# Performance work log

Hardware: AMD Instinct MI355X
Metric: run time of the kernel (lower is better)

## Reference

```python
import jax, jax.numpy as jnp
import numpy as np

N, E, IN_DIM, HID, H, D = 50000, 800000, 1280, 256, 4, 64  # gat_out_dim = H*D = HID
NEG_SLOPE = 0.2


def setup_inputs() -> dict:
    key = jax.random.key(0)
    ks = jax.random.split(key, 20)

    def lin(k, fi, fo):
        return (jax.random.normal(k, (fi, fo), jnp.float32) / np.float32(np.sqrt(fi)))

    inp = {
        "x": jax.random.normal(ks[0], (N, IN_DIM), jnp.float32),
        "edge_index": jax.random.randint(ks[1], (2, E), 0, N, dtype=jnp.int32),
        "enc_W": lin(ks[2], IN_DIM, HID), "enc_b": jnp.zeros((HID,), jnp.float32),
        "Wl0": lin(ks[3], HID, H * D), "bl0": jnp.zeros((H * D,), jnp.float32),
        "Wr0": lin(ks[4], HID, H * D), "br0": jnp.zeros((H * D,), jnp.float32),
        "att0": jax.random.normal(ks[5], (H, D), jnp.float32) / np.float32(np.sqrt(D)),
        "bias0": jnp.zeros((H * D,), jnp.float32),
        "Wl1": lin(ks[6], HID, H * D), "bl1": jnp.zeros((H * D,), jnp.float32),
        "Wr1": lin(ks[7], HID, H * D), "br1": jnp.zeros((H * D,), jnp.float32),
        "att1": jax.random.normal(ks[8], (H, D), jnp.float32) / np.float32(np.sqrt(D)),
        "bias1": jnp.zeros((H * D,), jnp.float32),
        "clf_W": lin(ks[9], HID, 1), "clf_b": jnp.zeros((1,), jnp.float32),
    }
    return inp


def gatv2_layer(x, src, dst, Wl, bl, Wr, br, att, bias):
    # x: [N, HID]; src/dst: [E'] with self-loops already appended
    xl = (x @ Wl + bl).reshape(N, H, D)  # source transform
    xr = (x @ Wr + br).reshape(N, H, D)  # target transform
    e = jax.nn.leaky_relu(xl[src] + xr[dst], NEG_SLOPE)   # [E', H, D]
    logits = jnp.einsum('ehd,hd->eh', e, att)              # [E', H]
    # segment softmax over destination nodes (every node has a self-loop)
    m = jax.ops.segment_max(logits, dst, num_segments=N)   # [N, H]
    a = jnp.exp(logits - m[dst])
    denom = jax.ops.segment_sum(a, dst, num_segments=N)
    alpha = a / (denom[dst] + 1e-16)                       # [E', H]
    out = jax.ops.segment_sum(xl[src] * alpha[:, :, None], dst, num_segments=N)
    out = out.reshape(N, H * D) + bias
    out = out + x  # residual (in_dim == out_features -> identity residual); dropout is eval-mode no-op
    return jax.nn.elu(out), alpha


def reference(x, edge_index, enc_W, enc_b, Wl0, bl0, Wr0, br0, att0, bias0,
              Wl1, bl1, Wr1, br1, att1, bias1, clf_W, clf_b):
    # add self loops (PyG GATv2Conv default)
    loops = jnp.arange(N, dtype=edge_index.dtype)
    src = jnp.concatenate([edge_index[0], loops])
    dst = jnp.concatenate([edge_index[1], loops])

    h = x @ enc_W + enc_b                                  # node encoder [N, HID]
    h, alpha0 = gatv2_layer(h, src, dst, Wl0, bl0, Wr0, br0, att0, bias0)
    h, alpha1 = gatv2_layer(h, src, dst, Wl1, bl1, Wr1, br1, att1, bias1)
    preds = (h @ clf_W + clf_b).squeeze(-1)                # [N]
    return preds, alpha0, alpha1
```

## Files before the change

### kernel.cpp

```cpp
#include <hip/hip_runtime.h>
#include <hip/hip_bf16.h>
#include <math.h>

#define N_NODES 50000
#define E_EDGES 800000
#define EP (E_EDGES + N_NODES)
#define IN_DIM 1280
#define HID 256
#define NHEAD 4
#define DHEAD 64
#define NEG_SLOPE 0.2f

typedef unsigned short ushort_t;
typedef __attribute__((ext_vector_type(8))) short short8;
typedef __attribute__((ext_vector_type(4))) float floatx4;

__device__ __forceinline__ void split_bf16(float x, ushort_t& hi, ushort_t& lo) {
  unsigned u = __float_as_uint(x);
  hi = (ushort_t)(u >> 16);
  float rem = x - __uint_as_float(u & 0xFFFF0000u);
  lo = (ushort_t)(__float_as_uint(rem) >> 16);
}

__device__ __forceinline__ void gload_lds16(const void* g, void* l) {
  __builtin_amdgcn_global_load_lds(
      (const __attribute__((address_space(1))) unsigned int*)g,
      (__attribute__((address_space(3))) unsigned int*)l, 16, 0, 0);
}


__global__ void hist_kernel(const int* __restrict__ ei, int* __restrict__ deg) {
  int e = blockIdx.x * blockDim.x + threadIdx.x;
  if (e >= EP) return;
  int dst = (e < E_EDGES) ? ei[E_EDGES + e] : (e - E_EDGES);
  atomicAdd(&deg[dst], 1);
}

__global__ __launch_bounds__(1024) void scan_kernel(int* __restrict__ dc, int* __restrict__ row_ptr) {
  __shared__ int wsum[16];
  int tid = threadIdx.x;
  int lane = tid & 63;
  int wid = tid >> 6;
  int running = 0;
  if (tid == 0) row_ptr[0] = 0;
  for (int base = 0; base < N_NODES; base += 1024) {
    int i = base + tid;
    int v = (i < N_NODES) ? dc[i] : 0;
    int s = v;
    #pragma unroll
    for (int off = 1; off < 64; off <<= 1) {
      int t = __shfl_up(s, off);
      if (lane >= off) s += t;
    }
    if (lane == 63) wsum[wid] = s;
    __syncthreads();
    if (wid == 0 && lane < 16) {
      int w = wsum[lane];
      #pragma unroll
      for (int off = 1; off < 16; off <<= 1) {
        int t = __shfl_up(w, off);
        if (lane >= off) w += t;
      }
      wsum[lane] = w;
    }
    __syncthreads();
    int woff = (wid > 0) ? wsum[wid - 1] : 0;
    int incl = running + woff + s;
    if (i < N_NODES) {
      row_ptr[i + 1] = incl;
      dc[i] = incl - v;
    }
    running += wsum[15];
    __syncthreads();
  }
}

__global__ void scatter_kernel(const int* __restrict__ ei, int* __restrict__ cursor,
                               int* __restrict__ csr_src, int* __restrict__ csr_eid) {
  int e = blockIdx.x * blockDim.x + threadIdx.x;
  if (e >= EP) return;
  int src, dst;
  if (e < E_EDGES) { src = ei[e]; dst = ei[E_EDGES + e]; }
  else             { src = dst = e - E_EDGES; }
  int pos = atomicAdd(&cursor[dst], 1);
  csr_src[pos] = src;
  csr_eid[pos] = e;
}

__global__ void wsplit_packed(const float* __restrict__ W, ushort_t* __restrict__ Ph,
                              ushort_t* __restrict__ Pl, int K, int Nc, int NcT, int colOff) {
  int idx = blockIdx.x * blockDim.x + threadIdx.x;
  if (idx >= K * Nc) return;
  int k = idx / Nc, n = idx - k * Nc;
  ushort_t hi, lo;
  split_bf16(W[idx], hi, lo);
  size_t pi = ((size_t)(k >> 3) * NcT + colOff + n) * 8 + (k & 7);
  Ph[pi] = hi;
  Pl[pi] = lo;
}

__device__ __forceinline__ void split_store16(const float* va, ushort_t* dAh,
                                              ushort_t* dAl, int awoff) {
  #pragma unroll
  for (int hh = 0; hh < 2; ++hh) {
    short8 hv, lv;
    #pragma unroll
    for (int i = 0; i < 8; ++i) {
      ushort_t hi, lo;
      split_bf16(va[hh * 8 + i], hi, lo);
      hv[i] = (short)hi; lv[i] = (short)lo;
    }
    *(short8*)&dAh[awoff + hh * 8] = hv;
    *(short8*)&dAl[awoff + hh * 8] = lv;
  }
}

__global__ __launch_bounds__(256, 2) void gemm128(const float* __restrict__ A,
                                                  const ushort_t* __restrict__ Bh,
                                                  const ushort_t* __restrict__ Bl,
                                                  const float* __restrict__ bias_l,
                                                  const float* __restrict__ bias_r,
                                                  float* __restrict__ C_l,
                                                  float* __restrict__ C_r,
                                                  int M, int K, int NcT, int Nsplit) {
  __shared__ ushort_t sAh[2][128 * 40];
  __shared__ ushort_t sAl[2][128 * 40];
  __shared__ ushort_t sBh[2][128 * 32];
  __shared__ ushort_t sBl[2][128 * 32];

  const int P = NcT >> 7;
  const int plog = (P == 2) ? 1 : 2;
  const int id = blockIdx.x;
  const int xcd = id & 7;
  const int kk = id >> 3;
  const int cpan = kk & (P - 1);
  const int Rhi = kk >> plog;
  const int R = (Rhi << 3) + xcd;
  const int MBp = (M + 127) >> 7;
  if (R >= MBp) return;

  const int tid = threadIdx.x;
  const int lane = tid & 63;
  const int w = tid >> 6;
  const int wm = w >> 1, wn = w & 1;
  const int bm = R * 128;
  const int bn = cpan * 128;
  const int r = lane & 15, q = lane >> 4;

  floatx4 acc[4][4];
  #pragma unroll
  for (int i = 0; i < 4; ++i)
    #pragma unroll
    for (int j = 0; j < 4; ++j) acc[i][j] = (floatx4)(0.0f);

  const int arow = tid >> 1, achunk = tid & 1;
  int ag = bm + arow; if (ag >= M) ag = M - 1;
  const float* aptr = A + (size_t)ag * K + achunk * 16;
  const int awoff = arow * 40 + achunk * 16;

  const int e0 = tid, e1 = tid + 256;
  const size_t b0base = ((size_t)(e0 >> 7) * NcT + bn + (e0 & 127)) * 8;
  const size_t b1base = ((size_t)(e1 >> 7) * NcT + bn + (e1 & 127)) * 8;

  const int nt = K >> 5;

  {
    gload_lds16(Bh + b0base, &sBh[0][e0 * 8]);
    gload_lds16(Bh + b1base, &sBh[0][e1 * 8]);
    gload_lds16(Bl + b0base, &sBl[0][e0 * 8]);
    gload_lds16(Bl + b1base, &sBl[0][e1 * 8]);
    float va[16];
    *(float4*)&va[0]  = *(const float4*)(aptr + 0);
    *(float4*)&va[4]  = *(const float4*)(aptr + 4);
    *(float4*)&va[8]  = *(const float4*)(aptr + 8);
    *(float4*)&va[12] = *(const float4*)(aptr + 12);
    split_store16(va, sAh[0], sAl[0], awoff);
  }
  __syncthreads();

  int cur = 0;
  for (int t = 0; t < nt; ++t) {
    const bool has_next = (t + 1 < nt);
    float va[16];
    if (has_next) {
      const int k0n = (t + 1) << 5;
      *(float4*)&va[0]  = *(const float4*)(aptr + k0n + 0);
      *(float4*)&va[4]  = *(const float4*)(aptr + k0n + 4);
      *(float4*)&va[8]  = *(const float4*)(aptr + k0n + 8);
      *(float4*)&va[12] = *(const float4*)(aptr + k0n + 12);
      size_t kadd = (size_t)(k0n >> 3) * NcT * 8;
      gload_lds16(Bh + b0base + kadd, &sBh[cur ^ 1][e0 * 8]);
      gload_lds16(Bh + b1base + kadd, &sBh[cur ^ 1][e1 * 8]);
      gload_lds16(Bl + b0base + kadd, &sBl[cur ^ 1][e0 * 8]);
      gload_lds16(Bl + b1base + kadd, &sBl[cur ^ 1][e1 * 8]);
    }

    short8 ah[4], al[4];
    #pragma unroll
    for (int i = 0; i < 4; ++i) {
      int off = (wm * 64 + i * 16 + r) * 40 + q * 8;
      ah[i] = *(const short8*)&sAh[cur][off];
      al[i] = *(const short8*)&sAl[cur][off];
    }
    #pragma unroll
    for (int j = 0; j < 4; ++j) {
      int off = (q * 128 + wn * 64 + j * 16 + r) * 8;
      short8 bh = *(const short8*)&sBh[cur][off];
      short8 bl = *(const short8*)&sBl[cur][off];
      #pragma unroll
      for (int i = 0; i < 4; ++i) {
        acc[i][j] = __builtin_amdgcn_mfma_f32_16x16x32_bf16(ah[i], bh, acc[i][j], 0, 0, 0);
        acc[i][j] = __builtin_amdgcn_mfma_f32_16x16x32_bf16(ah[i], bl, acc[i][j], 0, 0, 0);
        acc[i][j] = __builtin_amdgcn_mfma_f32_16x16x32_bf16(al[i], bh, acc[i][j], 0, 0, 0);
      }
    }

    if (has_next) split_store16(va, sAh[cur ^ 1], sAl[cur ^ 1], awoff);

    __syncthreads();
    cur ^= 1;
  }

  #pragma unroll
  for (int j = 0; j < 4; ++j) {
    int cg = bn + wn * 64 + j * 16 + r;
    bool sec = cg >= Nsplit;
    int cc = sec ? cg - Nsplit : cg;
    float bv = sec ? bias_r[cc] : bias_l[cc];
    float* Cb = sec ? C_r : C_l;
    #pragma unroll
    for (int i = 0; i < 4; ++i) {
      int row0 = bm + wm * 64 + i * 16 + q * 4;
      #pragma unroll
      for (int rr = 0; rr < 4; ++rr) {
        int row = row0 + rr;
        if (row < M) Cb[(size_t)row * HID + cc] = acc[i][j][rr] + bv;
      }
    }
  }
}

__global__ __launch_bounds__(256) void gat_layer(const float* __restrict__ xl,
                                                 const float* __restrict__ xr,
                                                 float* h_inout,
                                                 const float* __restrict__ att,
                                                 const float* __restrict__ bias,
                                                 const int* __restrict__ row_ptr,
                                                 const int* __restrict__ csr_src,
                                                 const int* __restrict__ csr_eid,
                                                 float* __restrict__ logits_ws,
                                                 float* __restrict__ alpha_out) {
  int node = blockIdx.x * 4 + (threadIdx.x >> 6);
  int l = threadIdx.x & 63;
  int hgrp = l >> 4;
  int r0 = row_ptr[node];
  int r1 = row_ptr[node + 1];

  float4 xr4 = *(const float4*)(xr + (size_t)node * HID + l * 4);
  float4 at4 = *(const float4*)(att + l * 4);

  float m = -INFINITY;
  float den = 0.f;
  float4 acc = make_float4(0.f, 0.f, 0.f, 0.f);
  for (int j = r0; j < r1; ++j) {
    int s = csr_src[j];
    float4 v = *(const float4*)(xl + (size_t)s * HID + l * 4);
    float t0 = v.x + xr4.x; t0 = (t0 > 0.f) ? t0 : NEG_SLOPE * t0;
    float t1 = v.y + xr4.y; t1 = (t1 > 0.f) ? t1 : NEG_SLOPE * t1;
    float t2 = v.z + xr4.z; t2 = (t2 > 0.f) ? t2 : NEG_SLOPE * t2;
    float t3 = v.w + xr4.w; t3 = (t3 > 0.f) ? t3 : NEG_SLOPE * t3;
    float p = t0 * at4.x + t1 * at4.y + t2 * at4.z + t3 * at4.w;
    p += __shfl_xor(p, 1);
    p += __shfl_xor(p, 2);
    p += __shfl_xor(p, 4);
    p += __shfl_xor(p, 8);
    if ((l & 15) == 0) logits_ws[(size_t)j * NHEAD + hgrp] = p;
    float m_new = fmaxf(m, p);
    float scale = __expf(m - m_new);
    float wgt = __expf(p - m_new);
    den = den * scale + wgt;
    acc.x = acc.x * scale + wgt * v.x;
    acc.y = acc.y * scale + wgt * v.y;
    acc.z = acc.z * scale + wgt * v.z;
    acc.w = acc.w * scale + wgt * v.w;
    m = m_new;
  }
  float inv_den = 1.f / (den + 1e-16f);

  float4 b4 = *(const float4*)(bias + l * 4);
  float4 h4 = *(const float4*)(h_inout + (size_t)node * HID + l * 4);
  float o0 = acc.x * inv_den + b4.x + h4.x;
  float o1 = acc.y * inv_den + b4.y + h4.y;
  float o2 = acc.z * inv_den + b4.z + h4.z;
  float o3 = acc.w * inv_den + b4.w + h4.w;
  o0 = (o0 > 0.f) ? o0 : (__expf(o0) - 1.f);
  o1 = (o1 > 0.f) ? o1 : (__expf(o1) - 1.f);
  o2 = (o2 > 0.f) ? o2 : (__expf(o2) - 1.f);
  o3 = (o3 > 0.f) ? o3 : (__expf(o3) - 1.f);
  *(float4*)(h_inout + (size_t)node * HID + l * 4) = make_float4(o0, o1, o2, o3);

  __threadfence_block();

  float mh = __shfl(m, (l & 3) * 16);
  float dh = __shfl(den, (l & 3) * 16);
  float invd = 1.f / (dh + 1e-16f);
  for (int j = r0 + (l >> 2); j < r1; j += 16) {
    float lg = logits_ws[(size_t)j * NHEAD + (l & 3)];
    alpha_out[(size_t)csr_eid[j] * NHEAD + (l & 3)] = __expf(lg - mh) * invd;
  }
}

__global__ __launch_bounds__(64) void clf_kernel(const float* __restrict__ h,
                                                 const float* __restrict__ clf_W,
                                                 const float* __restrict__ clf_b,
                                                 float* __restrict__ preds) {
  int n = blockIdx.x;
  int l = threadIdx.x;
  float4 v = *(const float4*)(h + (size_t)n * HID + l * 4);
  float4 w = *(const float4*)(clf_W + l * 4);
  float s = v.x * w.x + v.y * w.y + v.z * w.z + v.w * w.w;
  s += __shfl_xor(s, 1);
  s += __shfl_xor(s, 2);
  s += __shfl_xor(s, 4);
  s += __shfl_xor(s, 8);
  s += __shfl_xor(s, 16);
  s += __shfl_xor(s, 32);
  if (l == 0) preds[n] = s + clf_b[0];
}

static inline char* carve(char*& p, size_t bytes) {
  char* ret = p;
  p += (bytes + 255) & ~(size_t)255;
  return ret;
}

extern "C" void kernel_launch(void* const* d_in, const int* in_sizes, int n_in,
                              void* d_out, int out_size, void* d_ws, size_t ws_size,
                              hipStream_t stream) {
  const float* x     = (const float*)d_in[0];
  const int*   ei    = (const int*)d_in[1];
  const float* enc_W = (const float*)d_in[2];
  const float* enc_b = (const float*)d_in[3];
  const float* Wl0   = (const float*)d_in[4];
  const float* bl0   = (const float*)d_in[5];
  const float* Wr0   = (const float*)d_in[6];
  const float* br0   = (const float*)d_in[7];
  const float* att0  = (const float*)d_in[8];
  const float* bias0 = (const float*)d_in[9];
  const float* Wl1   = (const float*)d_in[10];
  const float* bl1   = (const float*)d_in[11];
  const float* Wr1   = (const float*)d_in[12];
  const float* br1   = (const float*)d_in[13];
  const float* att1  = (const float*)d_in[14];
  const float* bias1 = (const float*)d_in[15];
  const float* clf_W = (const float*)d_in[16];
  const float* clf_b = (const float*)d_in[17];

  float* preds  = (float*)d_out;
  float* alpha0 = preds + N_NODES;
  float* alpha1 = alpha0 + (size_t)EP * NHEAD;

  char* p = (char*)d_ws;
  float* h      = (float*)carve(p, (size_t)N_NODES * HID * 4);
  float* xl     = (float*)carve(p, (size_t)N_NODES * HID * 4);
  float* xr     = (float*)carve(p, (size_t)N_NODES * HID * 4);
  float* logits = (float*)carve(p, (size_t)EP * NHEAD * 4);
  int* row_ptr  = (int*)carve(p, (size_t)(N_NODES + 1) * 4);
  int* cursor   = (int*)carve(p, (size_t)N_NODES * 4);
  int* csr_src  = (int*)carve(p, (size_t)EP * 4);
  int* csr_eid  = (int*)carve(p, (size_t)EP * 4);
  ushort_t* encPh = (ushort_t*)carve(p, (size_t)IN_DIM * HID * 2);
  ushort_t* encPl = (ushort_t*)carve(p, (size_t)IN_DIM * HID * 2);
  ushort_t* P0h   = (ushort_t*)carve(p, (size_t)HID * 512 * 2);
  ushort_t* P0l   = (ushort_t*)carve(p, (size_t)HID * 512 * 2);
  ushort_t* P1h   = (ushort_t*)carve(p, (size_t)HID * 512 * 2);
  ushort_t* P1l   = (ushort_t*)carve(p, (size_t)HID * 512 * 2);

  hipMemsetAsync(cursor, 0, N_NODES * sizeof(int), stream);
  int eb = 256, eg = (EP + eb - 1) / eb;
  hist_kernel<<<eg, eb, 0, stream>>>(ei, cursor);
  scan_kernel<<<1, 1024, 0, stream>>>(cursor, row_ptr);
  scatter_kernel<<<eg, eb, 0, stream>>>(ei, cursor, csr_src, csr_eid);

  int wt = 256;
  wsplit_packed<<<(IN_DIM * HID + wt - 1) / wt, wt, 0, stream>>>(enc_W, encPh, encPl, IN_DIM, HID, HID, 0);
  wsplit_packed<<<(HID * HID + wt - 1) / wt, wt, 0, stream>>>(Wl0, P0h, P0l, HID, HID, 512, 0);
  wsplit_packed<<<(HID * HID + wt - 1) / wt, wt, 0, stream>>>(Wr0, P0h, P0l, HID, HID, 512, 256);
  wsplit_packed<<<(HID * HID + wt - 1) / wt, wt, 0, stream>>>(Wl1, P1h, P1l, HID, HID, 512, 0);
  wsplit_packed<<<(HID * HID + wt - 1) / wt, wt, 0, stream>>>(Wr1, P1h, P1l, HID, HID, 512, 256);

  const int MB = (N_NODES + 127) / 128;
  const int R8 = (MB + 7) / 8;
  dim3 bGemm(256);

  gemm128<<<dim3(8 * 2 * R8), bGemm, 0, stream>>>(x, encPh, encPl, enc_b, enc_b, h, h,
                                                  N_NODES, IN_DIM, HID, HID);

  gemm128<<<dim3(8 * 4 * R8), bGemm, 0, stream>>>(h, P0h, P0l, bl0, br0, xl, xr,
                                                  N_NODES, HID, 512, HID);
  gat_layer<<<N_NODES / 4, 256, 0, stream>>>(xl, xr, h, att0, bias0, row_ptr, csr_src, csr_eid, logits, alpha0);

  gemm128<<<dim3(8 * 4 * R8), bGemm, 0, stream>>>(h, P1h, P1l, bl1, br1, xl, xr,
                                                  N_NODES, HID, 512, HID);
  gat_layer<<<N_NODES / 4, 256, 0, stream>>>(xl, xr, h, att1, bias1, row_ptr, csr_src, csr_eid, logits, alpha1);

  clf_kernel<<<N_NODES, 64, 0, stream>>>(h, clf_W, clf_b, preds);
}
```

Before: 1.085 ms.

## Merge weight-split launches, prefetch gather rows, fuse classifier into GAT layer

Combines the five weight-splitting launches into one kernel that picks its matrix from the flat index. The GAT edge loop now loads source rows two at a time with the next pair prefetched, so gather latency overlaps the softmax math. The classifier dot product moves into the second GAT layer's epilogue, removing a separate launch and a re-read of h. It also drops the __threadfence_block before the alpha pass, which relies on the same wave reading back its own logits writes.

```diff
diff --git a/kernel.cpp b/kernel.cpp
--- a/kernel.cpp
+++ b/kernel.cpp
@@ -87,13 +87,31 @@
   csr_eid[pos] = e;
 }
 
-__global__ void wsplit_packed(const float* __restrict__ W, ushort_t* __restrict__ Ph,
-                              ushort_t* __restrict__ Pl, int K, int Nc, int NcT, int colOff) {
+#define ENC_ELEMS (IN_DIM * HID)
+#define LYR_ELEMS (HID * HID)
+__global__ void wsplit_all(const float* __restrict__ enc_W,
+                           const float* __restrict__ Wl0, const float* __restrict__ Wr0,
+                           const float* __restrict__ Wl1, const float* __restrict__ Wr1,
+                           ushort_t* __restrict__ encPh, ushort_t* __restrict__ encPl,
+                           ushort_t* __restrict__ P0h, ushort_t* __restrict__ P0l,
+                           ushort_t* __restrict__ P1h, ushort_t* __restrict__ P1l) {
   int idx = blockIdx.x * blockDim.x + threadIdx.x;
-  if (idx >= K * Nc) return;
-  int k = idx / Nc, n = idx - k * Nc;
+  const float* W; ushort_t *Ph, *Pl; int NcT, colOff, r;
+  if (idx < ENC_ELEMS) {
+    W = enc_W; Ph = encPh; Pl = encPl; NcT = HID; colOff = 0; r = idx;
+  } else {
+    int q = idx - ENC_ELEMS;
+    int mId = q >> 16;
+    if (mId >= 4) return;
+    r = q & 0xFFFF;
+    W  = (mId == 0) ? Wl0 : (mId == 1) ? Wr0 : (mId == 2) ? Wl1 : Wr1;
+    Ph = (mId < 2) ? P0h : P1h;
+    Pl = (mId < 2) ? P0l : P1l;
+    NcT = 512; colOff = (mId & 1) * 256;
+  }
+  int k = r >> 8, n = r & 255;
   ushort_t hi, lo;
-  split_bf16(W[idx], hi, lo);
+  split_bf16(W[r], hi, lo);
   size_t pi = ((size_t)(k >> 3) * NcT + colOff + n) * 8 + (k & 7);
   Ph[pi] = hi;
   Pl[pi] = lo;
@@ -249,7 +267,10 @@
                                                  const int* __restrict__ csr_src,
                                                  const int* __restrict__ csr_eid,
                                                  float* __restrict__ logits_ws,
-                                                 float* __restrict__ alpha_out) {
+                                                 float* __restrict__ alpha_out,
+                                                 const float* __restrict__ clf_W,
+                                                 const float* __restrict__ clf_b,
+                                                 float* __restrict__ preds) {
   int node = blockIdx.x * 4 + (threadIdx.x >> 6);
   int l = threadIdx.x & 63;
   int hgrp = l >> 4;
@@ -262,9 +283,8 @@
   float m = -INFINITY;
   float den = 0.f;
   float4 acc = make_float4(0.f, 0.f, 0.f, 0.f);
-  for (int j = r0; j < r1; ++j) {
-    int s = csr_src[j];
-    float4 v = *(const float4*)(xl + (size_t)s * HID + l * 4);
+
+  auto process = [&](const float4& v, int j) {
     float t0 = v.x + xr4.x; t0 = (t0 > 0.f) ? t0 : NEG_SLOPE * t0;
     float t1 = v.y + xr4.y; t1 = (t1 > 0.f) ? t1 : NEG_SLOPE * t1;
     float t2 = v.z + xr4.z; t2 = (t2 > 0.f) ? t2 : NEG_SLOPE * t2;
@@ -284,6 +304,26 @@
     acc.z = acc.z * scale + wgt * v.z;
     acc.w = acc.w * scale + wgt * v.w;
     m = m_new;
+  };
+
+  float4 v0, v1;
+  {
+    int s0 = csr_src[r0];
+    int s1 = (r0 + 1 < r1) ? csr_src[r0 + 1] : s0;
+    v0 = *(const float4*)(xl + (size_t)s0 * HID + l * 4);
+    v1 = *(const float4*)(xl + (size_t)s1 * HID + l * 4);
+  }
+  for (int j = r0; j < r1; j += 2) {
+    float4 w0 = v0, w1 = v1;
+    int jn = j + 2;
+    if (jn < r1) {
+      int t0 = csr_src[jn];
+      int t1 = (jn + 1 < r1) ? csr_src[jn + 1] : t0;
+      v0 = *(const float4*)(xl + (size_t)t0 * HID + l * 4);
+      v1 = *(const float4*)(xl + (size_t)t1 * HID + l * 4);
+    }
+    process(w0, j);
+    if (j + 1 < r1) process(w1, j + 1);
   }
   float inv_den = 1.f / (den + 1e-16f);
 
@@ -299,7 +339,17 @@
   o3 = (o3 > 0.f) ? o3 : (__expf(o3) - 1.f);
   *(float4*)(h_inout + (size_t)node * HID + l * 4) = make_float4(o0, o1, o2, o3);
 
-  __threadfence_block();
+  if (preds != nullptr) {
+    float4 cw = *(const float4*)(clf_W + l * 4);
+    float s = o0 * cw.x + o1 * cw.y + o2 * cw.z + o3 * cw.w;
+    s += __shfl_xor(s, 1);
+    s += __shfl_xor(s, 2);
+    s += __shfl_xor(s, 4);
+    s += __shfl_xor(s, 8);
+    s += __shfl_xor(s, 16);
+    s += __shfl_xor(s, 32);
+    if (l == 0) preds[node] = s + clf_b[0];
+  }
 
   float mh = __shfl(m, (l & 3) * 16);
   float dh = __shfl(den, (l & 3) * 16);
@@ -308,24 +358,6 @@
     float lg = logits_ws[(size_t)j * NHEAD + (l & 3)];
     alpha_out[(size_t)csr_eid[j] * NHEAD + (l & 3)] = __expf(lg - mh) * invd;
   }
-}
-
-__global__ __launch_bounds__(64) void clf_kernel(const float* __restrict__ h,
-                                                 const float* __restrict__ clf_W,
-                                                 const float* __restrict__ clf_b,
-                                                 float* __restrict__ preds) {
-  int n = blockIdx.x;
-  int l = threadIdx.x;
-  float4 v = *(const float4*)(h + (size_t)n * HID + l * 4);
-  float4 w = *(const float4*)(clf_W + l * 4);
-  float s = v.x * w.x + v.y * w.y + v.z * w.z + v.w * w.w;
-  s += __shfl_xor(s, 1);
-  s += __shfl_xor(s, 2);
-  s += __shfl_xor(s, 4);
-  s += __shfl_xor(s, 8);
-  s += __shfl_xor(s, 16);
-  s += __shfl_xor(s, 32);
-  if (l == 0) preds[n] = s + clf_b[0];
 }
 
 static inline char* carve(char*& p, size_t bytes) {
@@ -382,12 +414,11 @@
   scan_kernel<<<1, 1024, 0, stream>>>(cursor, row_ptr);
   scatter_kernel<<<eg, eb, 0, stream>>>(ei, cursor, csr_src, csr_eid);
 
-  int wt = 256;
-  wsplit_packed<<<(IN_DIM * HID + wt - 1) / wt, wt, 0, stream>>>(enc_W, encPh, encPl, IN_DIM, HID, HID, 0);
-  wsplit_packed<<<(HID * HID + wt - 1) / wt, wt, 0, stream>>>(Wl0, P0h, P0l, HID, HID, 512, 0);
-  wsplit_packed<<<(HID * HID + wt - 1) / wt, wt, 0, stream>>>(Wr0, P0h, P0l, HID, HID, 512, 256);
-  wsplit_packed<<<(HID * HID + wt - 1) / wt, wt, 0, stream>>>(Wl1, P1h, P1l, HID, HID, 512, 0);
-  wsplit_packed<<<(HID * HID + wt - 1) / wt, wt, 0, stream>>>(Wr1, P1h, P1l, HID, HID, 512, 256);
+  {
+    const int total = ENC_ELEMS + 4 * LYR_ELEMS;
+    wsplit_all<<<(total + 255) / 256, 256, 0, stream>>>(enc_W, Wl0, Wr0, Wl1, Wr1,
+                                                        encPh, encPl, P0h, P0l, P1h, P1l);
+  }
 
   const int MB = (N_NODES + 127) / 128;
   const int R8 = (MB + 7) / 8;
@@ -398,11 +429,11 @@
 
   gemm128<<<dim3(8 * 4 * R8), bGemm, 0, stream>>>(h, P0h, P0l, bl0, br0, xl, xr,
                                                   N_NODES, HID, 512, HID);
-  gat_layer<<<N_NODES / 4, 256, 0, stream>>>(xl, xr, h, att0, bias0, row_ptr, csr_src, csr_eid, logits, alpha0);
+  gat_layer<<<N_NODES / 4, 256, 0, stream>>>(xl, xr, h, att0, bias0, row_ptr, csr_src,
+                                             csr_eid, logits, alpha0, nullptr, nullptr, nullptr);
 
   gemm128<<<dim3(8 * 4 * R8), bGemm, 0, stream>>>(h, P1h, P1l, bl1, br1, xl, xr,
                                                   N_NODES, HID, 512, HID);
-  gat_layer<<<N_NODES / 4, 256, 0, stream>>>(xl, xr, h, att1, bias1, row_ptr, csr_src, csr_eid, logits, alpha1);
-
-  clf_kernel<<<N_NODES, 64, 0, stream>>>(h, clf_W, clf_b, preds);
-}
+  gat_layer<<<N_NODES / 4, 256, 0, stream>>>(xl, xr, h, att1, bias1, row_ptr, csr_src,
+                                             csr_eid, logits, alpha1, clf_W, clf_b, preds);
+}
```

Result: faster. 1.055 ms (-2.8%).
